# Performance work log

Hardware: AMD Instinct MI355X
Metric: run time of the kernel (lower is better)

The kernel has to match this reference:

```python
import jax, jax.numpy as jnp
import numpy as np

B, N, C = 16, 1024, 768
E, H, D, K = 8, 192, 4, 2


def setup_inputs() -> dict:
    key = jax.random.key(0)
    ks = jax.random.split(key, 8)
    std = 0.02
    return {
        "x": jax.random.normal(ks[0], (B, N, C), jnp.float32),
        "task_ids": jax.random.randint(ks[1], (B,), 0, D),
        "eps": jax.random.normal(ks[2], (B, N, E), jnp.float32),
        "gate_w": jax.random.normal(ks[3], (D, C, 2 * E), jnp.float32) * std,
        "fc1_w": jax.random.normal(ks[4], (E, H, C), jnp.float32) * std,
        "fc1_b": jnp.zeros((E, H), jnp.float32),
        "fc2_w": jax.random.normal(ks[5], (E, C, H), jnp.float32) * std,
        "fc2_b": jnp.zeros((E, C), jnp.float32),
    }


def reference(x, task_ids, eps, gate_w, fc1_w, fc1_b, fc2_w, fc2_b):
    # per-sample gate selected by domain/task id: [B,N,2E]
    total_w = jnp.einsum("bnc,bce->bne", x, gate_w[task_ids])
    clean_logits, raw_noise = jnp.split(total_w, 2, axis=-1)  # [B,N,E] each
    noise_stddev = jax.nn.softplus(raw_noise) + 0.01
    logits = clean_logits + eps * noise_stddev  # [B,N,E]
    exp_wise_sum = logits.sum(axis=1)  # [B,E]

    top_k_logits, top_k_idx = jax.lax.top_k(exp_wise_sum, K)  # [B,K]
    m1 = top_k_logits.min(axis=1, keepdims=True)
    m2 = top_k_logits.max(axis=1, keepdims=True)
    scaled = (top_k_logits - m1) / (m2 - m1 + 1e-6)
    top_k_gates = jax.nn.softmax(scaled, axis=1)  # [B,K]

    gates_full = jnp.zeros((B, E), x.dtype).at[
        jnp.arange(B)[:, None], top_k_idx
    ].set(top_k_gates)  # [B,E]

    # dense all-expert adapter compute (faithful to original torch.stack)
    h = jnp.einsum("bnc,ehc->benh", x, fc1_w) + fc1_b[None, :, None, :]
    h = jax.nn.gelu(h, approximate=False)
    expert_outs = jnp.einsum("benh,ech->benc", h, fc2_w) + fc2_b[None, :, None, :]

    tot_x = jnp.einsum("be,benc->bnc", gates_full, expert_outs)
    return x + tot_x
```

## Files before the change

### kernel.cpp

```cpp
#include <hip/hip_runtime.h>

#define B_ 16
#define N_ 1024
#define C_ 768
#define E_ 8
#define H_ 192
#define K_ 2
#define GRID_ 512

typedef __bf16 bf16x8 __attribute__((ext_vector_type(8)));
typedef float  f32x4  __attribute__((ext_vector_type(4)));

__global__ __launch_bounds__(256) void prep_kernel(
    const float* __restrict__ w1, const float* __restrict__ w2,
    const float* __restrict__ gw,
    __bf16* __restrict__ pw1, __bf16* __restrict__ pw2,
    float* __restrict__ gwT, unsigned int* __restrict__ ctrl) {
  if (blockIdx.x == 0 && threadIdx.x < 129) ctrl[threadIdx.x] = 0;

  int idx = blockIdx.x * 256 + threadIdx.x;
  const int nW4 = (E_ * H_ * C_) / 4;
  if (idx >= nW4) return;
  int flat = idx * 4;
  int e = flat / (H_ * C_);
  int r = flat - e * (H_ * C_);

  {
    float4 a = *(const float4*)(w1 + (size_t)flat);
    int n = r / C_;
    int c = r - n * C_;
    size_t o = ((size_t)(e * 24 + (c >> 5)) * 192 + n) * 32 + (c & 31);
    pw1[o + 0] = (__bf16)a.x; pw1[o + 1] = (__bf16)a.y;
    pw1[o + 2] = (__bf16)a.z; pw1[o + 3] = (__bf16)a.w;
  }
  {
    float4 a = *(const float4*)(w2 + (size_t)flat);
    int n = r / H_;
    int h = r - n * H_;
    size_t o = ((size_t)(e * 6 + (h >> 5)) * 768 + n) * 32 + (h & 31);
    pw2[o + 0] = (__bf16)a.x; pw2[o + 1] = (__bf16)a.y;
    pw2[o + 2] = (__bf16)a.z; pw2[o + 3] = (__bf16)a.w;
  }
  if (idx < (4 * 16 * C_) / 4) {
    int f = idx * 4;
    int d = f / (16 * C_);
    int rr = f - d * (16 * C_);
    int j = rr / C_;
    int c = rr - j * C_;
    const float* src = gw + (size_t)d * C_ * 16 + j;
    float4 v;
    v.x = src[(size_t)(c + 0) * 16]; v.y = src[(size_t)(c + 1) * 16];
    v.z = src[(size_t)(c + 2) * 16]; v.w = src[(size_t)(c + 3) * 16];
    *(float4*)(gwT + (size_t)f) = v;
  }
}

__global__ __launch_bounds__(256, 2) void mega_kernel(
    const float* __restrict__ x, const int* __restrict__ task_ids,
    const float* __restrict__ eps, const float* __restrict__ gwT,
    const __bf16* __restrict__ pw1, const __bf16* __restrict__ pw2,
    const float* __restrict__ fc1_b, const float* __restrict__ fc2_b,
    float* __restrict__ sums, unsigned int* __restrict__ bar,
    float* __restrict__ out) {
  const int b = blockIdx.x & 15;
  const int tile = blockIdx.x >> 4;
  const int token0 = tile * 32;
  const int tid = threadIdx.x;

  __shared__ __align__(16) char smem[62464];
  float (*xt)[772]  = (float(*)[772])smem;
  float (*sc)[16]   = (float(*)[16])(smem + 49408);
  __bf16 (*xs)[776] = (__bf16(*)[776])smem;
  __bf16 (*hs)[200] = (__bf16(*)[200])(smem + 49664);

  {
    const int t = tid & 15;
    const int jg = tid >> 4;
    const int task = task_ids[b];
    const float* wrow = gwT + ((size_t)task * 16 + jg) * C_;
    float part = 0.0f;
#pragma unroll
    for (int pass = 0; pass < 2; ++pass) {
      const int tb = token0 + pass * 16;
      const float* xbase = x + ((size_t)b * N_ + tb) * C_;
      for (int it = 0; it < 12; ++it) {
        int chunk = it * 256 + tid;
        int row = chunk / 192;
        int col4 = chunk - row * 192;
        *(float4*)&xt[row][col4 * 4] =
            *(const float4*)(xbase + (size_t)row * C_ + col4 * 4);
      }
      __syncthreads();
      float acc = 0.0f;
#pragma unroll 4
      for (int c = 0; c < C_; c += 4) {
        float4 xv = *(const float4*)&xt[t][c];
        float4 wv = *(const float4*)(wrow + c);
        acc += xv.x * wv.x + xv.y * wv.y + xv.z * wv.z + xv.w * wv.w;
      }
      sc[t][jg] = acc;
      __syncthreads();
      if (jg < 8) {
        float clean = sc[t][jg];
        float raw = sc[t][jg + 8];
        float sp = (raw > 20.0f) ? raw : log1pf(expf(raw));
        part += clean + eps[((size_t)b * N_ + tb + t) * E_ + jg] * (sp + 0.01f);
      }
      __syncthreads();
    }
    if (jg < 8) sc[t][jg] = part;
    __syncthreads();
    if (tid < 8) {
      float s = 0.0f;
#pragma unroll
      for (int tt = 0; tt < 16; ++tt) s += sc[tt][tid];
      atomicAdd(&sums[b * E_ + tid], s);
    }
    __syncthreads();
  }

  if (tid == 0) {
    __threadfence();
    atomicAdd(bar, 1u);
    while (__hip_atomic_load(bar, __ATOMIC_ACQUIRE,
                             __HIP_MEMORY_SCOPE_AGENT) < (unsigned)GRID_)
      __builtin_amdgcn_s_sleep(8);
  }
  __syncthreads();

  int e_idx[2]; float gate_v[2];
  {
    float best = -INFINITY, best2 = -INFINITY;
    int i1 = 0, i2 = 0;
#pragma unroll
    for (int e = 0; e < E_; ++e) {
      float v = __hip_atomic_load(&sums[b * E_ + e], __ATOMIC_RELAXED,
                                  __HIP_MEMORY_SCOPE_AGENT);
      if (v > best) { best2 = best; i2 = i1; best = v; i1 = e; }
      else if (v > best2) { best2 = v; i2 = e; }
    }
    float d = best - best2;
    float st = d / (d + 1e-6f);
    float et = expf(st);
    e_idx[0] = i1; gate_v[0] = et / (et + 1.0f);
    e_idx[1] = i2; gate_v[1] = 1.0f / (et + 1.0f);
  }

  const int wave = tid >> 6;
  const int lane = tid & 63;
  const int ln = lane & 15;
  const int q8 = (lane >> 4) * 8;
  const int q4 = (lane >> 4) * 4;

  const float* xbase = x + ((size_t)b * N_ + token0) * C_;
  for (int it = 0; it < 12; ++it) {
    int chunk = it * 256 + tid;
    int row = chunk / 96;
    int col8 = chunk - row * 96;
    const float* p = xbase + (size_t)row * C_ + col8 * 8;
    float4 v0 = *(const float4*)p;
    float4 v1 = *(const float4*)(p + 4);
    bf16x8 t;
    t[0] = (__bf16)v0.x; t[1] = (__bf16)v0.y; t[2] = (__bf16)v0.z; t[3] = (__bf16)v0.w;
    t[4] = (__bf16)v1.x; t[5] = (__bf16)v1.y; t[6] = (__bf16)v1.z; t[7] = (__bf16)v1.w;
    *(bf16x8*)&xs[row][col8 * 8] = t;
  }
  __syncthreads();

  f32x4 c2[2][12] = {};

  for (int kx = 0; kx < 2; ++kx) {
    const int e = e_idx[kx];
    const float g = gate_v[kx];

    const __bf16* w1l = pw1 + (size_t)e * (24 * 192 * 32)
                            + (size_t)(wave * 48 + ln) * 32 + q8;
    bf16x8 bq[2][3], aq[2][2];
#pragma unroll
    for (int j = 0; j < 3; ++j) bq[0][j] = *(const bf16x8*)(w1l + j * 512);
    aq[0][0] = *(const bf16x8*)&xs[ln][q8];
    aq[0][1] = *(const bf16x8*)&xs[16 + ln][q8];
    f32x4 c1[2][3] = {};
#pragma unroll
    for (int kb = 0; kb < 24; ++kb) {
      int p = kb & 1;
      if (kb < 23) {
        const __bf16* nx = w1l + (size_t)(kb + 1) * 6144;
#pragma unroll
        for (int j = 0; j < 3; ++j) bq[p ^ 1][j] = *(const bf16x8*)(nx + j * 512);
        aq[p ^ 1][0] = *(const bf16x8*)&xs[ln][(kb + 1) * 32 + q8];
        aq[p ^ 1][1] = *(const bf16x8*)&xs[16 + ln][(kb + 1) * 32 + q8];
      }
#pragma unroll
      for (int j = 0; j < 3; ++j) {
        c1[0][j] = __builtin_amdgcn_mfma_f32_16x16x32_bf16(aq[p][0], bq[p][j], c1[0][j], 0, 0, 0);
        c1[1][j] = __builtin_amdgcn_mfma_f32_16x16x32_bf16(aq[p][1], bq[p][j], c1[1][j], 0, 0, 0);
      }
    }
#pragma unroll
    for (int j = 0; j < 3; ++j) {
      int col = wave * 48 + j * 16 + ln;
      float b1 = fc1_b[e * H_ + col];
#pragma unroll
      for (int m = 0; m < 2; ++m) {
#pragma unroll
        for (int r = 0; r < 4; ++r) {
          int row = m * 16 + q4 + r;
          float v = c1[m][j][r] + b1;
          float gl = 0.5f * v * (1.0f + erff(v * 0.70710678118f));
          hs[row][col] = (__bf16)(g * gl);
        }
      }
    }
    __syncthreads();

    const __bf16* w2l = pw2 + (size_t)e * (6 * 768 * 32)
                            + (size_t)(wave * 192 + ln) * 32 + q8;
    bf16x8 bh[2][6], av[2][2];
#pragma unroll
    for (int j = 0; j < 6; ++j) bh[0][j] = *(const bf16x8*)(w2l + j * 512);
    av[0][0] = *(const bf16x8*)&hs[ln][q8];
    av[0][1] = *(const bf16x8*)&hs[16 + ln][q8];
#pragma unroll
    for (int s = 0; s < 12; ++s) {
      const int kb = s >> 1;
      const int half = s & 1;
      const int p = s & 1;
      if (s < 11) {
        const int s2 = s + 1;
        const int kb2 = s2 >> 1;
        const int half2 = s2 & 1;
        const __bf16* src = w2l + (size_t)kb2 * 24576;
#pragma unroll
        for (int j = 0; j < 6; ++j)
          bh[p ^ 1][j] = *(const bf16x8*)(src + (half2 * 6 + j) * 512);
        if (half2 == 0) {
          av[kb2 & 1][0] = *(const bf16x8*)&hs[ln][kb2 * 32 + q8];
          av[kb2 & 1][1] = *(const bf16x8*)&hs[16 + ln][kb2 * 32 + q8];
        }
      }
#pragma unroll
      for (int j = 0; j < 6; ++j) {
        const int jj = half * 6 + j;
        c2[0][jj] = __builtin_amdgcn_mfma_f32_16x16x32_bf16(av[kb & 1][0], bh[p][j], c2[0][jj], 0, 0, 0);
        c2[1][jj] = __builtin_amdgcn_mfma_f32_16x16x32_bf16(av[kb & 1][1], bh[p][j], c2[1][jj], 0, 0, 0);
      }
    }
    __syncthreads();
  }

  const float* xr = x + ((size_t)b * N_ + token0) * C_;
  float* outr = out + ((size_t)b * N_ + token0) * C_;
#pragma unroll
  for (int j = 0; j < 12; ++j) {
    int col = wave * 192 + j * 16 + ln;
    float b2t = gate_v[0] * fc2_b[e_idx[0] * C_ + col] +
                gate_v[1] * fc2_b[e_idx[1] * C_ + col];
#pragma unroll
    for (int m = 0; m < 2; ++m) {
#pragma unroll
      for (int r = 0; r < 4; ++r) {
        int row = m * 16 + q4 + r;
        size_t off = (size_t)row * C_ + col;
        outr[off] = xr[off] + c2[m][j][r] + b2t;
      }
    }
  }
}

extern "C" void kernel_launch(void* const* d_in, const int* in_sizes, int n_in,
                              void* d_out, int out_size, void* d_ws, size_t ws_size,
                              hipStream_t stream) {
  const float* x      = (const float*)d_in[0];
  const int*   task   = (const int*)d_in[1];
  const float* eps    = (const float*)d_in[2];
  const float* gate_w = (const float*)d_in[3];
  const float* fc1_w  = (const float*)d_in[4];
  const float* fc1_b  = (const float*)d_in[5];
  const float* fc2_w  = (const float*)d_in[6];
  const float* fc2_b  = (const float*)d_in[7];
  float* out = (float*)d_out;

  const size_t nW = (size_t)E_ * H_ * C_;
  __bf16* pw1 = (__bf16*)d_ws;
  __bf16* pw2 = pw1 + nW;
  float* gwT  = (float*)((char*)d_ws + 2 * nW * sizeof(__bf16));
  float* sums = (float*)((char*)gwT + 4 * 16 * C_ * sizeof(float));
  unsigned int* bar = (unsigned int*)(sums + 128);

  prep_kernel<<<(nW / 4 + 255) / 256, 256, 0, stream>>>(
      fc1_w, fc2_w, gate_w, pw1, pw2, gwT, (unsigned int*)sums);
  mega_kernel<<<GRID_, 256, 0, stream>>>(x, task, eps, gwT, pw1, pw2,
                                         fc1_b, fc2_b, sums, bar, out);
}
```

Baseline: 237.0 us.

## Shrink LDS footprint, split K loads, and use per-batch barriers

The x staging for both the gate dot product and the fc1 MFMA is split into two K-halves, so the shared tile is half as wide and total LDS drops from about 62KB to about 50KB. Both experts' hidden activations are kept in shared memory at once, and fc2 is computed in two column halves so fewer accumulators are live. The grid-wide spin barrier becomes a per-batch barrier where each block waits only for the 32 blocks of its own sample. This adds extra syncthreads and more fc1 accumulators, and depends on the larger ctrl reset covering the per-batch counters.

```diff
diff --git a/kernel.cpp b/kernel.cpp
--- a/kernel.cpp
+++ b/kernel.cpp
@@ -16,7 +16,7 @@
     const float* __restrict__ gw,
     __bf16* __restrict__ pw1, __bf16* __restrict__ pw2,
     float* __restrict__ gwT, unsigned int* __restrict__ ctrl) {
-  if (blockIdx.x == 0 && threadIdx.x < 129) ctrl[threadIdx.x] = 0;
+  if (blockIdx.x == 0 && threadIdx.x < 144) ctrl[threadIdx.x] = 0;
 
   int idx = blockIdx.x * 256 + threadIdx.x;
   const int nW4 = (E_ * H_ * C_) / 4;
@@ -55,6 +55,13 @@
   }
 }
 
+__device__ __forceinline__ bf16x8 cvt8(const float4& a, const float4& b) {
+  bf16x8 t;
+  t[0] = (__bf16)a.x; t[1] = (__bf16)a.y; t[2] = (__bf16)a.z; t[3] = (__bf16)a.w;
+  t[4] = (__bf16)b.x; t[5] = (__bf16)b.y; t[6] = (__bf16)b.z; t[7] = (__bf16)b.w;
+  return t;
+}
+
 __global__ __launch_bounds__(256, 2) void mega_kernel(
     const float* __restrict__ x, const int* __restrict__ task_ids,
     const float* __restrict__ eps, const float* __restrict__ gwT,
@@ -67,11 +74,11 @@
   const int token0 = tile * 32;
   const int tid = threadIdx.x;
 
-  __shared__ __align__(16) char smem[62464];
-  float (*xt)[772]  = (float(*)[772])smem;
-  float (*sc)[16]   = (float(*)[16])(smem + 49408);
-  __bf16 (*xs)[776] = (__bf16(*)[776])smem;
-  __bf16 (*hs)[200] = (__bf16(*)[200])(smem + 49664);
+  __shared__ __align__(16) char smem[50688];
+  float (*xt)[388]  = (float(*)[388])smem;
+  float (*sc)[16]   = (float(*)[16])(smem + 24832);
+  __bf16 (*xs)[392] = (__bf16(*)[392])smem;
+  __bf16 (*hs)[32][200] = (__bf16(*)[32][200])(smem + 25088);
 
   {
     const int t = tid & 15;
@@ -83,20 +90,24 @@
     for (int pass = 0; pass < 2; ++pass) {
       const int tb = token0 + pass * 16;
       const float* xbase = x + ((size_t)b * N_ + tb) * C_;
-      for (int it = 0; it < 12; ++it) {
-        int chunk = it * 256 + tid;
-        int row = chunk / 192;
-        int col4 = chunk - row * 192;
-        *(float4*)&xt[row][col4 * 4] =
-            *(const float4*)(xbase + (size_t)row * C_ + col4 * 4);
-      }
-      __syncthreads();
       float acc = 0.0f;
+#pragma unroll
+      for (int kh = 0; kh < 2; ++kh) {
+        for (int it = 0; it < 6; ++it) {
+          int chunk = it * 256 + tid;
+          int row = chunk / 96;
+          int col4 = chunk - row * 96;
+          *(float4*)&xt[row][col4 * 4] =
+              *(const float4*)(xbase + (size_t)row * C_ + kh * 384 + col4 * 4);
+        }
+        __syncthreads();
 #pragma unroll 4
-      for (int c = 0; c < C_; c += 4) {
-        float4 xv = *(const float4*)&xt[t][c];
-        float4 wv = *(const float4*)(wrow + c);
-        acc += xv.x * wv.x + xv.y * wv.y + xv.z * wv.z + xv.w * wv.w;
+        for (int c = 0; c < 384; c += 4) {
+          float4 xv = *(const float4*)&xt[t][c];
+          float4 wv = *(const float4*)(wrow + kh * 384 + c);
+          acc += xv.x * wv.x + xv.y * wv.y + xv.z * wv.z + xv.w * wv.w;
+        }
+        __syncthreads();
       }
       sc[t][jg] = acc;
       __syncthreads();
@@ -121,9 +132,9 @@
 
   if (tid == 0) {
     __threadfence();
-    atomicAdd(bar, 1u);
-    while (__hip_atomic_load(bar, __ATOMIC_ACQUIRE,
-                             __HIP_MEMORY_SCOPE_AGENT) < (unsigned)GRID_)
+    atomicAdd(&bar[b], 1u);
+    while (__hip_atomic_load(&bar[b], __ATOMIC_ACQUIRE,
+                             __HIP_MEMORY_SCOPE_AGENT) < 32u)
       __builtin_amdgcn_s_sleep(8);
   }
   __syncthreads();
@@ -151,52 +162,54 @@
   const int ln = lane & 15;
   const int q8 = (lane >> 4) * 8;
   const int q4 = (lane >> 4) * 4;
-
   const float* xbase = x + ((size_t)b * N_ + token0) * C_;
-  for (int it = 0; it < 12; ++it) {
-    int chunk = it * 256 + tid;
-    int row = chunk / 96;
-    int col8 = chunk - row * 96;
-    const float* p = xbase + (size_t)row * C_ + col8 * 8;
-    float4 v0 = *(const float4*)p;
-    float4 v1 = *(const float4*)(p + 4);
-    bf16x8 t;
-    t[0] = (__bf16)v0.x; t[1] = (__bf16)v0.y; t[2] = (__bf16)v0.z; t[3] = (__bf16)v0.w;
-    t[4] = (__bf16)v1.x; t[5] = (__bf16)v1.y; t[6] = (__bf16)v1.z; t[7] = (__bf16)v1.w;
-    *(bf16x8*)&xs[row][col8 * 8] = t;
-  }
-  __syncthreads();
-
-  f32x4 c2[2][12] = {};
-
+
+  f32x4 c1[2][2][3] = {};
+#pragma unroll
+  for (int kh = 0; kh < 2; ++kh) {
+    __syncthreads();
+    for (int it = 0; it < 6; ++it) {
+      int chunk = it * 256 + tid;
+      int row = chunk / 48;
+      int col8 = chunk - row * 48;
+      const float* p = xbase + (size_t)row * C_ + kh * 384 + col8 * 8;
+      float4 v0 = *(const float4*)p;
+      float4 v1 = *(const float4*)(p + 4);
+      *(bf16x8*)&xs[row][col8 * 8] = cvt8(v0, v1);
+    }
+    __syncthreads();
+#pragma unroll
+    for (int kx = 0; kx < 2; ++kx) {
+      const __bf16* w1l = pw1 + (size_t)e_idx[kx] * 147456
+                              + (size_t)(kh * 12) * 6144
+                              + (size_t)(wave * 48 + ln) * 32 + q8;
+      bf16x8 bq[2][3], aq[2][2];
+#pragma unroll
+      for (int j = 0; j < 3; ++j) bq[0][j] = *(const bf16x8*)(w1l + j * 512);
+      aq[0][0] = *(const bf16x8*)&xs[ln][q8];
+      aq[0][1] = *(const bf16x8*)&xs[16 + ln][q8];
+#pragma unroll
+      for (int kb = 0; kb < 12; ++kb) {
+        int p = kb & 1;
+        if (kb < 11) {
+          const __bf16* nx = w1l + (size_t)(kb + 1) * 6144;
+#pragma unroll
+          for (int j = 0; j < 3; ++j) bq[p ^ 1][j] = *(const bf16x8*)(nx + j * 512);
+          aq[p ^ 1][0] = *(const bf16x8*)&xs[ln][(kb + 1) * 32 + q8];
+          aq[p ^ 1][1] = *(const bf16x8*)&xs[16 + ln][(kb + 1) * 32 + q8];
+        }
+#pragma unroll
+        for (int j = 0; j < 3; ++j) {
+          c1[kx][0][j] = __builtin_amdgcn_mfma_f32_16x16x32_bf16(aq[p][0], bq[p][j], c1[kx][0][j], 0, 0, 0);
+          c1[kx][1][j] = __builtin_amdgcn_mfma_f32_16x16x32_bf16(aq[p][1], bq[p][j], c1[kx][1][j], 0, 0, 0);
+        }
+      }
+    }
+  }
+#pragma unroll
   for (int kx = 0; kx < 2; ++kx) {
     const int e = e_idx[kx];
     const float g = gate_v[kx];
-
-    const __bf16* w1l = pw1 + (size_t)e * (24 * 192 * 32)
-                            + (size_t)(wave * 48 + ln) * 32 + q8;
-    bf16x8 bq[2][3], aq[2][2];
-#pragma unroll
-    for (int j = 0; j < 3; ++j) bq[0][j] = *(const bf16x8*)(w1l + j * 512);
-    aq[0][0] = *(const bf16x8*)&xs[ln][q8];
-    aq[0][1] = *(const bf16x8*)&xs[16 + ln][q8];
-    f32x4 c1[2][3] = {};
-#pragma unroll
-    for (int kb = 0; kb < 24; ++kb) {
-      int p = kb & 1;
-      if (kb < 23) {
-        const __bf16* nx = w1l + (size_t)(kb + 1) * 6144;
-#pragma unroll
-        for (int j = 0; j < 3; ++j) bq[p ^ 1][j] = *(const bf16x8*)(nx + j * 512);
-        aq[p ^ 1][0] = *(const bf16x8*)&xs[ln][(kb + 1) * 32 + q8];
-        aq[p ^ 1][1] = *(const bf16x8*)&xs[16 + ln][(kb + 1) * 32 + q8];
-      }
-#pragma unroll
-      for (int j = 0; j < 3; ++j) {
-        c1[0][j] = __builtin_amdgcn_mfma_f32_16x16x32_bf16(aq[p][0], bq[p][j], c1[0][j], 0, 0, 0);
-        c1[1][j] = __builtin_amdgcn_mfma_f32_16x16x32_bf16(aq[p][1], bq[p][j], c1[1][j], 0, 0, 0);
-      }
-    }
 #pragma unroll
     for (int j = 0; j < 3; ++j) {
       int col = wave * 48 + j * 16 + ln;
@@ -206,63 +219,70 @@
 #pragma unroll
         for (int r = 0; r < 4; ++r) {
           int row = m * 16 + q4 + r;
-          float v = c1[m][j][r] + b1;
+          float v = c1[kx][m][j][r] + b1;
           float gl = 0.5f * v * (1.0f + erff(v * 0.70710678118f));
-          hs[row][col] = (__bf16)(g * gl);
-        }
-      }
-    }
-    __syncthreads();
-
-    const __bf16* w2l = pw2 + (size_t)e * (6 * 768 * 32)
-                            + (size_t)(wave * 192 + ln) * 32 + q8;
-    bf16x8 bh[2][6], av[2][2];
-#pragma unroll
-    for (int j = 0; j < 6; ++j) bh[0][j] = *(const bf16x8*)(w2l + j * 512);
-    av[0][0] = *(const bf16x8*)&hs[ln][q8];
-    av[0][1] = *(const bf16x8*)&hs[16 + ln][q8];
-#pragma unroll
-    for (int s = 0; s < 12; ++s) {
-      const int kb = s >> 1;
-      const int half = s & 1;
-      const int p = s & 1;
-      if (s < 11) {
-        const int s2 = s + 1;
-        const int kb2 = s2 >> 1;
-        const int half2 = s2 & 1;
-        const __bf16* src = w2l + (size_t)kb2 * 24576;
-#pragma unroll
-        for (int j = 0; j < 6; ++j)
-          bh[p ^ 1][j] = *(const bf16x8*)(src + (half2 * 6 + j) * 512);
-        if (half2 == 0) {
-          av[kb2 & 1][0] = *(const bf16x8*)&hs[ln][kb2 * 32 + q8];
-          av[kb2 & 1][1] = *(const bf16x8*)&hs[16 + ln][kb2 * 32 + q8];
-        }
-      }
-#pragma unroll
-      for (int j = 0; j < 6; ++j) {
-        const int jj = half * 6 + j;
-        c2[0][jj] = __builtin_amdgcn_mfma_f32_16x16x32_bf16(av[kb & 1][0], bh[p][j], c2[0][jj], 0, 0, 0);
-        c2[1][jj] = __builtin_amdgcn_mfma_f32_16x16x32_bf16(av[kb & 1][1], bh[p][j], c2[1][jj], 0, 0, 0);
-      }
-    }
-    __syncthreads();
-  }
+          hs[kx][row][col] = (__bf16)(g * gl);
+        }
+      }
+    }
+  }
+  __syncthreads();
 
   const float* xr = x + ((size_t)b * N_ + token0) * C_;
   float* outr = out + ((size_t)b * N_ + token0) * C_;
 #pragma unroll
-  for (int j = 0; j < 12; ++j) {
-    int col = wave * 192 + j * 16 + ln;
-    float b2t = gate_v[0] * fc2_b[e_idx[0] * C_ + col] +
-                gate_v[1] * fc2_b[e_idx[1] * C_ + col];
-#pragma unroll
-    for (int m = 0; m < 2; ++m) {
-#pragma unroll
-      for (int r = 0; r < 4; ++r) {
-        int row = m * 16 + q4 + r;
-        size_t off = (size_t)row * C_ + col;
-        outr[off] = xr[off] + c2[m][j][r] + b2t;
+  for (int half = 0; half < 2; ++half) {
+    const int colbase = wave * 192 + half * 96;
+    f32x4 c2[2][6] = {};
+#pragma unroll
+    for (int kx = 0; kx < 2; ++kx) {
+      const __bf16(*hse)[200] = hs[kx];
+      const __bf16* w2l = pw2 + (size_t)e_idx[kx] * 147456
+                              + (size_t)(colbase + ln) * 32 + q8;
+      bf16x8 bh[2][3], av[2][2];
+#pragma unroll
+      for (int j = 0; j < 3; ++j) bh[0][j] = *(const bf16x8*)(w2l + j * 512);
+      av[0][0] = *(const bf16x8*)&hse[ln][q8];
+      av[0][1] = *(const bf16x8*)&hse[16 + ln][q8];
+#pragma unroll
+      for (int s = 0; s < 12; ++s) {
+        const int kb = s >> 1;
+        const int sub = s & 1;
+        const int p = s & 1;
+        if (s < 11) {
+          const int s2 = s + 1;
+          const int kb2 = s2 >> 1;
+          const int sub2 = s2 & 1;
+          const __bf16* src = w2l + (size_t)kb2 * 24576;
+#pragma unroll
+          for (int j = 0; j < 3; ++j)
+            bh[p ^ 1][j] = *(const bf16x8*)(src + (sub2 * 3 + j) * 512);
+          if (sub2 == 0) {
+            av[kb2 & 1][0] = *(const bf16x8*)&hse[ln][kb2 * 32 + q8];
+            av[kb2 & 1][1] = *(const bf16x8*)&hse[16 + ln][kb2 * 32 + q8];
+          }
+        }
+#pragma unroll
+        for (int j = 0; j < 3; ++j) {
+          const int jj = sub * 3 + j;
+          c2[0][jj] = __builtin_amdgcn_mfma_f32_16x16x32_bf16(av[kb & 1][0], bh[p][j], c2[0][jj], 0, 0, 0);
+          c2[1][jj] = __builtin_amdgcn_mfma_f32_16x16x32_bf16(av[kb & 1][1], bh[p][j], c2[1][jj], 0, 0, 0);
+        }
+      }
+    }
+#pragma unroll
+    for (int j = 0; j < 6; ++j) {
+      int col = colbase + j * 16 + ln;
+      float b2t = gate_v[0] * fc2_b[e_idx[0] * C_ + col] +
+                  gate_v[1] * fc2_b[e_idx[1] * C_ + col];
+#pragma unroll
+      for (int m = 0; m < 2; ++m) {
+#pragma unroll
+        for (int r = 0; r < 4; ++r) {
+          int row = m * 16 + q4 + r;
+          size_t off = (size_t)row * C_ + col;
+          outr[off] = xr[off] + c2[m][j][r] + b2t;
+        }
       }
     }
   }
```

New measurement: 239.8 us. No clear change (+1.2%).
